# Kernel optimization log

Hardware: AMD Instinct MI355X
Metric: run time of the kernel (lower is better)

The kernel has to match this reference:

```python
import jax, jax.numpy as jnp
import numpy as np

N_NODES = 50000
N_EDGES = 1600000
N_GRAPHS = 64
IN_DIM = 128
HID = 128
N_CLASSES = 10


def setup_inputs() -> dict:
    key = jax.random.key(0)
    ks = jax.random.split(key, 12)
    x = jax.random.normal(ks[0], (N_NODES, IN_DIM), dtype=jnp.float32)
    edge_index = jax.random.randint(ks[1], (2, N_EDGES), 0, N_NODES, dtype=jnp.int32)
    batch = jnp.sort(jax.random.randint(ks[2], (N_NODES,), 0, N_GRAPHS, dtype=jnp.int32))
    def glorot(k, shape):
        s = 1.0 / np.sqrt(shape[0])
        return jax.random.uniform(k, shape, jnp.float32, -s, s)
    W1 = glorot(ks[3], (IN_DIM, HID)); b1 = jnp.zeros((HID,), jnp.float32)
    W2 = glorot(ks[4], (HID, HID));    b2 = jnp.zeros((HID,), jnp.float32)
    Wc1 = glorot(ks[5], (HID, HID));   bc1 = glorot(ks[6], (HID,))
    Wc2 = glorot(ks[7], (HID, N_CLASSES)); bc2 = glorot(ks[8], (N_CLASSES,))
    return {"x": x, "edge_index": edge_index, "batch": batch,
            "W1": W1, "b1": b1, "W2": W2, "b2": b2,
            "Wc1": Wc1, "bc1": bc1, "Wc2": Wc2, "bc2": bc2}


def gcn_conv(x, edge_index, W, b):
    """PyG GCNConv: sym-normalized A-hat (with self loops) @ (x W) + b."""
    n = x.shape[0]
    loop = jnp.arange(n, dtype=edge_index.dtype)
    src = jnp.concatenate([edge_index[0], loop])  # message source
    dst = jnp.concatenate([edge_index[1], loop])  # message target
    deg = jax.ops.segment_sum(jnp.ones_like(src, dtype=x.dtype), dst, num_segments=n)
    dinv = jnp.where(deg > 0, jax.lax.rsqrt(deg), jnp.zeros_like(deg))
    norm = dinv[src] * dinv[dst]  # [E+N]
    h = x @ W                     # [N, H]
    msg = h[src] * norm[:, None]  # gather + scale
    out = jax.ops.segment_sum(msg, dst, num_segments=n)
    return out + b


def reference(x, edge_index, batch, W1, b1, W2, b2, Wc1, bc1, Wc2, bc2):
    h = jax.nn.relu(gcn_conv(x, edge_index, W1, b1))
    h = jax.nn.relu(gcn_conv(h, edge_index, W2, b2))
    # per-graph mean pooling (segment mean)
    sums = jax.ops.segment_sum(h, batch, num_segments=N_GRAPHS)
    cnt = jax.ops.segment_sum(jnp.ones((h.shape[0],), h.dtype), batch, num_segments=N_GRAPHS)
    g = sums / jnp.clip(cnt, 1.0)[:, None]  # [G, H]
    z = jax.nn.relu(g @ Wc1 + bc1)
    return z @ Wc2 + bc2
```

## Files before the change

### kernel.cpp

```cpp
#include <hip/hip_runtime.h>
#include <cstdint>
#include <cstddef>

#define CHUNK 4096

typedef __attribute__((ext_vector_type(8))) short short8;
typedef __attribute__((ext_vector_type(4))) float f32x4;

__device__ __forceinline__ float bf2f(unsigned short u) {
  return __uint_as_float(((unsigned)u) << 16);
}
__device__ __forceinline__ unsigned short f2bf(float f) {
  unsigned u = __float_as_uint(f);
  u += 0x7fffu + ((u >> 16) & 1u);
  return (unsigned short)(u >> 16);
}

__global__ void transpose2_w_k(const float* __restrict__ W1, const float* __restrict__ W2,
                               unsigned short* __restrict__ W1t, unsigned short* __restrict__ W2t) {
  int idx = blockIdx.x * 256 + threadIdx.x;
  const float* W = (idx < 16384) ? W1 : W2;
  unsigned short* Wt = (idx < 16384) ? W1t : W2t;
  int i = idx & 16383;
  int k = i >> 7, n = i & 127;
  Wt[n * 128 + k] = f2bf(W[i]);
}

__global__ void count_edges_k(const int* __restrict__ dst, int E, int* __restrict__ cnt) {
  int e = blockIdx.x * blockDim.x + threadIdx.x;
  if (e < E) atomicAdd(&cnt[dst[e]], 1);
}

__global__ void dinv_k(const int* __restrict__ cnt, float* __restrict__ dinv, int n) {
  int i = blockIdx.x * blockDim.x + threadIdx.x;
  if (i < n) dinv[i] = rsqrtf((float)cnt[i] + 1.0f);
}

template <typename CT>
__global__ void fill_csr_k(const int* __restrict__ src, const int* __restrict__ dst, int E,
                           int* __restrict__ cursor, CT* __restrict__ col) {
  int e = blockIdx.x * blockDim.x + threadIdx.x;
  if (e < E) {
    int d = dst[e], s = src[e];
    int pos = atomicAdd(&cursor[d], 1);
    col[pos] = (CT)s;
  }
}

__global__ void scan1_k(const int* __restrict__ cnt, int* __restrict__ rs,
                        int* __restrict__ partials, int n) {
  __shared__ int s[1024];
  int t = threadIdx.x;
  int gid = blockIdx.x * 1024 + t;
  int v = (gid < n) ? cnt[gid] : 0;
  s[t] = v;
  __syncthreads();
  for (int off = 1; off < 1024; off <<= 1) {
    int u = (t >= off) ? s[t - off] : 0;
    __syncthreads();
    s[t] += u;
    __syncthreads();
  }
  if (gid < n) rs[gid] = s[t] - v;
  if (t == 1023) partials[blockIdx.x] = s[1023];
}

__global__ void scan2_k(int* __restrict__ partials, int nb) {
  if (threadIdx.x == 0 && blockIdx.x == 0) {
    int acc = 0;
    for (int i = 0; i < nb; i++) { int v = partials[i]; partials[i] = acc; acc += v; }
  }
}

__global__ void scan3_k(int* __restrict__ rs, int* __restrict__ cursor,
                        const int* __restrict__ partials, int n, int total) {
  int gid = blockIdx.x * blockDim.x + threadIdx.x;
  if (gid < n) {
    int v = rs[gid] + partials[gid >> 10];
    rs[gid] = v;
    cursor[gid] = v;
  }
  if (gid == 0) rs[n] = total;
}

__global__ __launch_bounds__(256) void scatter_atomic_k(const int* __restrict__ src,
                                                        const int* __restrict__ dst, int E,
                                                        int* __restrict__ gcur,
                                                        unsigned int* __restrict__ tmp,
                                                        int cap, int B) {
  __shared__ unsigned pk[CHUNK];
  __shared__ unsigned char bk[CHUNK];
  __shared__ int h[256];
  __shared__ int cur[256];
  __shared__ int base_s[256];
  int t = threadIdx.x;
  h[t] = 0;
  __syncthreads();
  int e0 = blockIdx.x * CHUNK;
  int e1 = e0 + CHUNK; if (e1 > E) e1 = E;
  int m = e1 - e0;
  for (int i = t; i < m; i += 256) {
    int d = dst[e0 + i], s = src[e0 + i];
    int b = d >> 8;
    pk[i] = ((unsigned)s << 8) | (unsigned)(d & 255);
    bk[i] = (unsigned char)b;
    atomicAdd(&h[b], 1);
  }
  __syncthreads();
  if (t < B && h[t] > 0) base_s[t] = atomicAdd(&gcur[t], h[t]);
  cur[t] = 0;
  __syncthreads();
  for (int i = t; i < m; i += 256) {
    int b = bk[i];
    int r = atomicAdd(&cur[b], 1);
    int p = base_s[b] + r;
    if (p < cap) tmp[(size_t)b * cap + p] = pk[i];
  }
}

__global__ void base2_k(const int* __restrict__ gcur, int B, int cap,
                        int* __restrict__ bucket_base) {
  int lane = threadIdx.x;
  int running = 0;
  for (int c0 = 0; c0 < B; c0 += 64) {
    int idx = c0 + lane;
    int cb = (idx < B) ? gcur[idx] : 0;
    if (cb > cap) cb = cap;
    int v = cb;
    #pragma unroll
    for (int off = 1; off < 64; off <<= 1) {
      int u = __shfl_up(v, off);
      if (lane >= off) v += u;
    }
    int tot = __shfl(v, 63);
    if (idx < B) bucket_base[idx] = running + (v - cb);
    running += tot;
  }
  if (lane == 0) bucket_base[B] = running;
}

__global__ __launch_bounds__(256) void cntfill2_k(const unsigned int* __restrict__ tmp,
                                                  const int* __restrict__ gcur,
                                                  const int* __restrict__ bucket_base,
                                                  int N, int E, int cap,
                                                  float* __restrict__ dinv,
                                                  int* __restrict__ rs,
                                                  unsigned short* __restrict__ col) {
  __shared__ int c[256];
  __shared__ int cur[256];
  int b = blockIdx.x, t = threadIdx.x;
  c[t] = 0;
  __syncthreads();
  int cnt_b = gcur[b]; if (cnt_b > cap) cnt_b = cap;
  const unsigned* tb = tmp + (size_t)b * cap;
  for (int i = t; i < cnt_b; i += 256) atomicAdd(&c[tb[i] & 255u], 1);
  __syncthreads();
  int v = c[t];
  cur[t] = v;
  __syncthreads();
  for (int off = 1; off < 256; off <<= 1) {
    int u = (t >= off) ? cur[t - off] : 0;
    __syncthreads();
    cur[t] += u;
    __syncthreads();
  }
  int rsv = bucket_base[b] + cur[t] - v;
  int node = (b << 8) + t;
  if (node < N) {
    rs[node] = rsv;
    dinv[node] = rsqrtf((float)v + 1.0f);
  }
  if (b == 0 && t == 0) rs[N] = E;
  __syncthreads();
  cur[t] = rsv;
  __syncthreads();
  for (int i = t; i < cnt_b; i += 256) {
    unsigned u = tb[i];
    int pos = atomicAdd(&cur[u & 255u], 1);
    col[pos] = (unsigned short)(u >> 8);
  }
}

template <bool AF32>
__global__ __launch_bounds__(256) void gemm_bf_k(const void* __restrict__ Ap,
                                                 const unsigned short* __restrict__ Wt,
                                                 unsigned short* __restrict__ C, int N) {
  __shared__ unsigned short Ws[128 * 136];
  for (int idx = threadIdx.x; idx < 2048; idx += 256) {
    int n = idx >> 4, c = idx & 15;
    *(uint4*)&Ws[n * 136 + c * 8] = ((const uint4*)Wt)[idx];
  }
  __syncthreads();
  const int w = threadIdx.x >> 6;
  const int lane = threadIdx.x & 63;
  const int quad = lane >> 4, l16 = lane & 15;
  const int rb = blockIdx.x * 128 + w * 32;
  f32x4 acc[2][8] = {};
  #pragma unroll
  for (int ks = 0; ks < 4; ks++) {
    short8 aF[2];
    #pragma unroll
    for (int m = 0; m < 2; m++) {
      int r = rb + m * 16 + l16;
      short8 a = {};
      if (r < N) {
        if (AF32) {
          const float* ar = (const float*)Ap + (size_t)r * 128 + ks * 32 + quad * 8;
          float4 u0 = *(const float4*)ar;
          float4 u1 = *(const float4*)(ar + 4);
          a[0] = (short)f2bf(u0.x); a[1] = (short)f2bf(u0.y);
          a[2] = (short)f2bf(u0.z); a[3] = (short)f2bf(u0.w);
          a[4] = (short)f2bf(u1.x); a[5] = (short)f2bf(u1.y);
          a[6] = (short)f2bf(u1.z); a[7] = (short)f2bf(u1.w);
        } else {
          a = *(const short8*)((const unsigned short*)Ap + (size_t)r * 128 + ks * 32 + quad * 8);
        }
      }
      aF[m] = a;
    }
    #pragma unroll
    for (int t = 0; t < 8; t++) {
      short8 bF = *(const short8*)&Ws[(t * 16 + l16) * 136 + ks * 32 + quad * 8];
      acc[0][t] = __builtin_amdgcn_mfma_f32_16x16x32_bf16(aF[0], bF, acc[0][t], 0, 0, 0);
      acc[1][t] = __builtin_amdgcn_mfma_f32_16x16x32_bf16(aF[1], bF, acc[1][t], 0, 0, 0);
    }
  }
  __syncthreads();
  unsigned short* Cs = Ws;
  #pragma unroll
  for (int m = 0; m < 2; m++) {
    int rloc = w * 32 + m * 16 + quad * 4;
    #pragma unroll
    for (int t = 0; t < 8; t++)
      #pragma unroll
      for (int rg = 0; rg < 4; rg++)
        Cs[(rloc + rg) * 132 + t * 16 + l16] = f2bf(acc[m][t][rg]);
  }
  __syncthreads();
  const int r0 = blockIdx.x * 128;
  for (int idx = threadIdx.x; idx < 2048; idx += 256) {
    int row = idx >> 4, c = idx & 15;
    int rr = r0 + row;
    if (rr < N) {
      uint2 a = *(uint2*)&Cs[row * 132 + c * 8];
      uint2 b = *(uint2*)&Cs[row * 132 + c * 8 + 4];
      ((uint4*)C)[(size_t)rr * 16 + c] = make_uint4(a.x, a.y, b.x, b.y);
    }
  }
}

template <typename CT>
__global__ __launch_bounds__(256) void agg8_k(const unsigned short* __restrict__ h,
                                              const int* __restrict__ rs,
                                              const CT* __restrict__ col,
                                              const float* __restrict__ dinv,
                                              const float* __restrict__ bias,
                                              unsigned short* __restrict__ outp, int n) {
  int wid = (blockIdx.x * blockDim.x + threadIdx.x) >> 6;
  int lane = threadIdx.x & 63;
  if (wid >= n) return;
  const int g = lane >> 4;
  const int l = lane & 15;
  float di = dinv[wid];
  float acc[8];
  {
    uint4 sv = ((const uint4*)(h + (size_t)wid * 128))[l];
    float ws = (g == 0) ? di : 0.f;
    acc[0] = bf2f((unsigned short)sv.x) * ws;
    acc[1] = bf2f((unsigned short)(sv.x >> 16)) * ws;
    acc[2] = bf2f((unsigned short)sv.y) * ws;
    acc[3] = bf2f((unsigned short)(sv.y >> 16)) * ws;
    acc[4] = bf2f((unsigned short)sv.z) * ws;
    acc[5] = bf2f((unsigned short)(sv.z >> 16)) * ws;
    acc[6] = bf2f((unsigned short)sv.w) * ws;
    acc[7] = bf2f((unsigned short)(sv.w >> 16)) * ws;
  }
  int beg = rs[wid], end = rs[wid + 1];
  for (int base = beg; base < end; base += 8) {
    int e0 = base + g, e1 = base + 4 + g;
    int i0 = (e0 < end) ? e0 : end - 1;
    int i1 = (e1 < end) ? e1 : end - 1;
    int s0 = (int)col[i0], s1 = (int)col[i1];
    float w0 = (e0 < end) ? dinv[s0] : 0.f;
    float w1 = (e1 < end) ? dinv[s1] : 0.f;
    uint4 h0 = ((const uint4*)(h + (size_t)s0 * 128))[l];
    uint4 h1 = ((const uint4*)(h + (size_t)s1 * 128))[l];
    acc[0] += bf2f((unsigned short)h0.x) * w0 + bf2f((unsigned short)h1.x) * w1;
    acc[1] += bf2f((unsigned short)(h0.x >> 16)) * w0 + bf2f((unsigned short)(h1.x >> 16)) * w1;
    acc[2] += bf2f((unsigned short)h0.y) * w0 + bf2f((unsigned short)h1.y) * w1;
    acc[3] += bf2f((unsigned short)(h0.y >> 16)) * w0 + bf2f((unsigned short)(h1.y >> 16)) * w1;
    acc[4] += bf2f((unsigned short)h0.z) * w0 + bf2f((unsigned short)h1.z) * w1;
    acc[5] += bf2f((unsigned short)(h0.z >> 16)) * w0 + bf2f((unsigned short)(h1.z >> 16)) * w1;
    acc[6] += bf2f((unsigned short)h0.w) * w0 + bf2f((unsigned short)h1.w) * w1;
    acc[7] += bf2f((unsigned short)(h0.w >> 16)) * w0 + bf2f((unsigned short)(h1.w >> 16)) * w1;
  }
  #pragma unroll
  for (int j = 0; j < 8; j++) {
    acc[j] += __shfl_xor(acc[j], 16);
    acc[j] += __shfl_xor(acc[j], 32);
  }
  if (g == 0) {
    float4 bA = *(const float4*)(bias + l * 8);
    float4 bB = *(const float4*)(bias + l * 8 + 4);
    float r0 = fmaxf(acc[0] * di + bA.x, 0.f);
    float r1 = fmaxf(acc[1] * di + bA.y, 0.f);
    float r2 = fmaxf(acc[2] * di + bA.z, 0.f);
    float r3 = fmaxf(acc[3] * di + bA.w, 0.f);
    float r4 = fmaxf(acc[4] * di + bB.x, 0.f);
    float r5 = fmaxf(acc[5] * di + bB.y, 0.f);
    float r6 = fmaxf(acc[6] * di + bB.z, 0.f);
    float r7 = fmaxf(acc[7] * di + bB.w, 0.f);
    uint4 v;
    v.x = (unsigned)f2bf(r0) | ((unsigned)f2bf(r1) << 16);
    v.y = (unsigned)f2bf(r2) | ((unsigned)f2bf(r3) << 16);
    v.z = (unsigned)f2bf(r4) | ((unsigned)f2bf(r5) << 16);
    v.w = (unsigned)f2bf(r6) | ((unsigned)f2bf(r7) << 16);
    ((uint4*)outp)[(size_t)wid * 16 + l] = v;
  }
}

__global__ void poolb_k(const unsigned short* __restrict__ h, const int* __restrict__ batch, int n,
                        float* __restrict__ pool, float* __restrict__ gcnt) {
  int f = threadIdx.x;
  int n0 = blockIdx.x * 64;
  if (n0 >= n) return;
  int n1 = n0 + 64; if (n1 > n) n1 = n;
  int gcur = batch[n0];
  float acc = 0.f, cacc = 0.f;
  for (int i = n0; i < n1; i++) {
    int g = batch[i];
    if (g != gcur) {
      atomicAdd(&pool[gcur * 128 + f], acc);
      if (f == 0) atomicAdd(&gcnt[gcur], cacc);
      acc = 0.f; cacc = 0.f; gcur = g;
    }
    acc += bf2f(h[(size_t)i * 128 + f]);
    cacc += 1.f;
  }
  atomicAdd(&pool[gcur * 128 + f], acc);
  if (f == 0) atomicAdd(&gcnt[gcur], cacc);
}

__global__ void classify_k(const float* __restrict__ pool, const float* __restrict__ gcnt,
                           const float* __restrict__ Wc1, const float* __restrict__ bc1,
                           const float* __restrict__ Wc2, const float* __restrict__ bc2,
                           float* __restrict__ out, int nc) {
  __shared__ float gs[128];
  __shared__ float zs[128];
  int g = blockIdx.x, t = threadIdx.x;
  float c = gcnt[g]; if (c < 1.f) c = 1.f;
  gs[t] = pool[g * 128 + t] / c;
  __syncthreads();
  float acc = bc1[t];
  for (int k = 0; k < 128; k++) acc += gs[k] * Wc1[k * 128 + t];
  zs[t] = fmaxf(acc, 0.f);
  __syncthreads();
  if (t < nc) {
    float o = bc2[t];
    for (int k = 0; k < 128; k++) o += zs[k] * Wc2[k * nc + t];
    out[g * nc + t] = o;
  }
}

extern "C" void kernel_launch(void* const* d_in, const int* in_sizes, int n_in,
                              void* d_out, int out_size, void* d_ws, size_t ws_size,
                              hipStream_t stream) {
  const float* x   = (const float*)d_in[0];
  const int*   ei  = (const int*)d_in[1];
  const int*   bat = (const int*)d_in[2];
  const float* W1  = (const float*)d_in[3];
  const float* b1  = (const float*)d_in[4];
  const float* W2  = (const float*)d_in[5];
  const float* b2  = (const float*)d_in[6];
  const float* Wc1 = (const float*)d_in[7];
  const float* bc1 = (const float*)d_in[8];
  const float* Wc2 = (const float*)d_in[9];
  const float* bc2 = (const float*)d_in[10];
  float* out = (float*)d_out;

  const int N  = in_sizes[0] / 128;
  const int E  = in_sizes[1] / 2;
  const int NC = in_sizes[10];
  const int G  = out_size / NC;
  const int* src = ei;
  const int* dst = ei + E;
  (void)n_in; (void)ws_size;

  size_t off = 0;
  auto walloc = [&](size_t bytes) -> void* {
    void* p = (char*)d_ws + off;
    off += (bytes + 255) & ~(size_t)255;
    return p;
  };
  unsigned short* B2 = (unsigned short*)walloc((size_t)N * 128 * 2);
  unsigned short* B3 = (unsigned short*)walloc((size_t)N * 128 * 2);
  unsigned short* W1t = (unsigned short*)walloc(128 * 128 * 2);
  unsigned short* W2t = (unsigned short*)walloc(128 * 128 * 2);
  float* dinv = (float*)walloc((size_t)N * 4);
  int*   rs   = (int*)  walloc((size_t)(N + 1) * 4);
  float* pool = (float*)walloc((size_t)G * 129 * 4);
  float* gcnt = pool + (size_t)G * 128;

  const bool small = (N <= 65535);
  const int gblocks = (N + 127) / 128;
  const int aggGrid = (N + 3) / 4;

  transpose2_w_k<<<128, 256, 0, stream>>>(W1, W2, W1t, W2t);

  if (small) {
    const int B    = (N + 255) >> 8;
    const int nblk = (E + CHUNK - 1) / CHUNK;
    const int cap  = (E + B - 1) / B + 2048;
    unsigned short* col = (unsigned short*)walloc((size_t)E * 2);
    unsigned int*   tmp = (unsigned int*)  walloc((size_t)B * cap * 4);
    int* gcur        = (int*)walloc((size_t)B * 4);
    int* bucket_base = (int*)walloc((size_t)(B + 1) * 4);

    hipMemsetAsync(gcur, 0, (size_t)B * 4, stream);
    scatter_atomic_k<<<nblk, 256, 0, stream>>>(src, dst, E, gcur, tmp, cap, B);
    base2_k<<<1, 64, 0, stream>>>(gcur, B, cap, bucket_base);
    cntfill2_k<<<B, 256, 0, stream>>>(tmp, gcur, bucket_base, N, E, cap, dinv, rs, col);

    gemm_bf_k<true><<<gblocks, 256, 0, stream>>>(x, W1t, B2, N);
    agg8_k<unsigned short><<<aggGrid, 256, 0, stream>>>(B2, rs, col, dinv, b1, B3, N);
    gemm_bf_k<false><<<gblocks, 256, 0, stream>>>(B3, W2t, B2, N);
    agg8_k<unsigned short><<<aggGrid, 256, 0, stream>>>(B2, rs, col, dinv, b2, B3, N);
  } else {
    const int nb = (N + 1023) / 1024;
    int* cnt    = (int*)walloc((size_t)N * 4);
    int* cursor = (int*)walloc((size_t)N * 4);
    int* col    = (int*)walloc((size_t)E * 4);
    int* partials = (int*)walloc(256 * 4);
    hipMemsetAsync(cnt, 0, (size_t)N * 4, stream);
    count_edges_k<<<(E + 255) / 256, 256, 0, stream>>>(dst, E, cnt);
    scan1_k<<<nb, 1024, 0, stream>>>(cnt, rs, partials, N);
    scan2_k<<<1, 64, 0, stream>>>(partials, nb);
    scan3_k<<<(N + 255) / 256, 256, 0, stream>>>(rs, cursor, partials, N, E);
    dinv_k<<<(N + 255) / 256, 256, 0, stream>>>(cnt, dinv, N);
    fill_csr_k<int><<<(E + 255) / 256, 256, 0, stream>>>(src, dst, E, cursor, col);

    gemm_bf_k<true><<<gblocks, 256, 0, stream>>>(x, W1t, B2, N);
    agg8_k<int><<<aggGrid, 256, 0, stream>>>(B2, rs, col, dinv, b1, B3, N);
    gemm_bf_k<false><<<gblocks, 256, 0, stream>>>(B3, W2t, B2, N);
    agg8_k<int><<<aggGrid, 256, 0, stream>>>(B2, rs, col, dinv, b2, B3, N);
  }

  hipMemsetAsync(pool, 0, (size_t)G * 129 * 4, stream);
  poolb_k<<<(N + 63) / 64, 128, 0, stream>>>(B3, bat, N, pool, gcnt);
  classify_k<<<G, 128, 0, stream>>>(pool, gcnt, Wc1, bc1, Wc2, bc2, out, NC);
}
```

Before: 314.4 us.

## Fuse CSR finalize, both GCN layers, pooling and classifier into one cooperative kernel

Replaces the chain of separate launches after edge bucketing (base scan, CSR fill, two GEMMs, two aggregations, pooling, classifier) with a single persistent cooperative kernel separated by grid-wide syncs. The weight transpose, bucket-counter reset and pool zeroing are folded into one prep kernel, replacing the memsets. The bucket-base scan is recomputed in every block. The aim is to remove launch overhead and inter-kernel gaps, at the cost of grid barriers and of grid-stride loops that may under-fill the device in some phases.

```diff
diff --git a/kernel.cpp b/kernel.cpp
--- a/kernel.cpp
+++ b/kernel.cpp
@@ -1,6 +1,9 @@
 #include <hip/hip_runtime.h>
+#include <hip/hip_cooperative_groups.h>
 #include <cstdint>
 #include <cstddef>
+
+namespace cg = cooperative_groups;
 
 #define CHUNK 4096
 
@@ -16,71 +19,18 @@
   return (unsigned short)(u >> 16);
 }
 
-__global__ void transpose2_w_k(const float* __restrict__ W1, const float* __restrict__ W2,
-                               unsigned short* __restrict__ W1t, unsigned short* __restrict__ W2t) {
+__global__ void prep_k(const float* __restrict__ W1, const float* __restrict__ W2,
+                       unsigned short* __restrict__ W1t, unsigned short* __restrict__ W2t,
+                       int* __restrict__ gcur, int B, float* __restrict__ pool, int poolN) {
   int idx = blockIdx.x * 256 + threadIdx.x;
   const float* W = (idx < 16384) ? W1 : W2;
   unsigned short* Wt = (idx < 16384) ? W1t : W2t;
   int i = idx & 16383;
   int k = i >> 7, n = i & 127;
   Wt[n * 128 + k] = f2bf(W[i]);
-}
-
-__global__ void count_edges_k(const int* __restrict__ dst, int E, int* __restrict__ cnt) {
-  int e = blockIdx.x * blockDim.x + threadIdx.x;
-  if (e < E) atomicAdd(&cnt[dst[e]], 1);
-}
-
-__global__ void dinv_k(const int* __restrict__ cnt, float* __restrict__ dinv, int n) {
-  int i = blockIdx.x * blockDim.x + threadIdx.x;
-  if (i < n) dinv[i] = rsqrtf((float)cnt[i] + 1.0f);
-}
-
-template <typename CT>
-__global__ void fill_csr_k(const int* __restrict__ src, const int* __restrict__ dst, int E,
-                           int* __restrict__ cursor, CT* __restrict__ col) {
-  int e = blockIdx.x * blockDim.x + threadIdx.x;
-  if (e < E) {
-    int d = dst[e], s = src[e];
-    int pos = atomicAdd(&cursor[d], 1);
-    col[pos] = (CT)s;
-  }
-}
-
-__global__ void scan1_k(const int* __restrict__ cnt, int* __restrict__ rs,
-                        int* __restrict__ partials, int n) {
-  __shared__ int s[1024];
-  int t = threadIdx.x;
-  int gid = blockIdx.x * 1024 + t;
-  int v = (gid < n) ? cnt[gid] : 0;
-  s[t] = v;
-  __syncthreads();
-  for (int off = 1; off < 1024; off <<= 1) {
-    int u = (t >= off) ? s[t - off] : 0;
-    __syncthreads();
-    s[t] += u;
-    __syncthreads();
-  }
-  if (gid < n) rs[gid] = s[t] - v;
-  if (t == 1023) partials[blockIdx.x] = s[1023];
-}
-
-__global__ void scan2_k(int* __restrict__ partials, int nb) {
-  if (threadIdx.x == 0 && blockIdx.x == 0) {
-    int acc = 0;
-    for (int i = 0; i < nb; i++) { int v = partials[i]; partials[i] = acc; acc += v; }
-  }
-}
-
-__global__ void scan3_k(int* __restrict__ rs, int* __restrict__ cursor,
-                        const int* __restrict__ partials, int n, int total) {
-  int gid = blockIdx.x * blockDim.x + threadIdx.x;
-  if (gid < n) {
-    int v = rs[gid] + partials[gid >> 10];
-    rs[gid] = v;
-    cursor[gid] = v;
-  }
-  if (gid == 0) rs[n] = total;
+  if (blockIdx.x == 0 && threadIdx.x < B) gcur[threadIdx.x] = 0;
+  if (blockIdx.x == 127)
+    for (int j = threadIdx.x; j < poolN; j += 256) pool[j] = 0.f;
 }
 
 __global__ __launch_bounds__(256) void scatter_atomic_k(const int* __restrict__ src,
@@ -118,83 +68,38 @@
   }
 }
 
-__global__ void base2_k(const int* __restrict__ gcur, int B, int cap,
-                        int* __restrict__ bucket_base) {
-  int lane = threadIdx.x;
-  int running = 0;
-  for (int c0 = 0; c0 < B; c0 += 64) {
-    int idx = c0 + lane;
-    int cb = (idx < B) ? gcur[idx] : 0;
-    if (cb > cap) cb = cap;
-    int v = cb;
-    #pragma unroll
-    for (int off = 1; off < 64; off <<= 1) {
-      int u = __shfl_up(v, off);
-      if (lane >= off) v += u;
-    }
-    int tot = __shfl(v, 63);
-    if (idx < B) bucket_base[idx] = running + (v - cb);
-    running += tot;
-  }
-  if (lane == 0) bucket_base[B] = running;
-}
-
-__global__ __launch_bounds__(256) void cntfill2_k(const unsigned int* __restrict__ tmp,
-                                                  const int* __restrict__ gcur,
-                                                  const int* __restrict__ bucket_base,
-                                                  int N, int E, int cap,
-                                                  float* __restrict__ dinv,
-                                                  int* __restrict__ rs,
-                                                  unsigned short* __restrict__ col) {
-  __shared__ int c[256];
-  __shared__ int cur[256];
-  int b = blockIdx.x, t = threadIdx.x;
-  c[t] = 0;
-  __syncthreads();
-  int cnt_b = gcur[b]; if (cnt_b > cap) cnt_b = cap;
-  const unsigned* tb = tmp + (size_t)b * cap;
-  for (int i = t; i < cnt_b; i += 256) atomicAdd(&c[tb[i] & 255u], 1);
-  __syncthreads();
-  int v = c[t];
-  cur[t] = v;
-  __syncthreads();
-  for (int off = 1; off < 256; off <<= 1) {
-    int u = (t >= off) ? cur[t - off] : 0;
-    __syncthreads();
-    cur[t] += u;
-    __syncthreads();
-  }
-  int rsv = bucket_base[b] + cur[t] - v;
-  int node = (b << 8) + t;
-  if (node < N) {
-    rs[node] = rsv;
-    dinv[node] = rsqrtf((float)v + 1.0f);
-  }
-  if (b == 0 && t == 0) rs[N] = E;
-  __syncthreads();
-  cur[t] = rsv;
-  __syncthreads();
-  for (int i = t; i < cnt_b; i += 256) {
-    unsigned u = tb[i];
-    int pos = atomicAdd(&cur[u & 255u], 1);
-    col[pos] = (unsigned short)(u >> 8);
-  }
-}
+struct CoopArgs {
+  const float* x;
+  const unsigned short* W1t; const unsigned short* W2t;
+  const float* b1; const float* b2;
+  const int* gcur; const unsigned* tmp; int cap; int B;
+  float* dinv; int* rs; unsigned short* col;
+  unsigned short* B2; unsigned short* B3;
+  const int* bat; float* pool; float* gcnt;
+  const float* Wc1; const float* bc1; const float* Wc2; const float* bc2;
+  float* out;
+  int N; int E; int NC; int G; int ntiles; int naggq;
+};
+
+union SMem {
+  unsigned short ws[128 * 136];
+  struct { int c[256]; int cur[256]; int sb[256]; } cf;
+  struct { float gs[128]; float zs[128]; } cl;
+};
 
 template <bool AF32>
-__global__ __launch_bounds__(256) void gemm_bf_k(const void* __restrict__ Ap,
-                                                 const unsigned short* __restrict__ Wt,
-                                                 unsigned short* __restrict__ C, int N) {
-  __shared__ unsigned short Ws[128 * 136];
+__device__ __forceinline__ void gemm_tile(SMem& sm, const void* Ap,
+                                          const unsigned short* Wt,
+                                          unsigned short* C, int N, int tile) {
   for (int idx = threadIdx.x; idx < 2048; idx += 256) {
     int n = idx >> 4, c = idx & 15;
-    *(uint4*)&Ws[n * 136 + c * 8] = ((const uint4*)Wt)[idx];
+    *(uint4*)&sm.ws[n * 136 + c * 8] = ((const uint4*)Wt)[idx];
   }
   __syncthreads();
   const int w = threadIdx.x >> 6;
   const int lane = threadIdx.x & 63;
   const int quad = lane >> 4, l16 = lane & 15;
-  const int rb = blockIdx.x * 128 + w * 32;
+  const int rb = tile * 128 + w * 32;
   f32x4 acc[2][8] = {};
   #pragma unroll
   for (int ks = 0; ks < 4; ks++) {
@@ -220,13 +125,13 @@
     }
     #pragma unroll
     for (int t = 0; t < 8; t++) {
-      short8 bF = *(const short8*)&Ws[(t * 16 + l16) * 136 + ks * 32 + quad * 8];
+      short8 bF = *(const short8*)&sm.ws[(t * 16 + l16) * 136 + ks * 32 + quad * 8];
       acc[0][t] = __builtin_amdgcn_mfma_f32_16x16x32_bf16(aF[0], bF, acc[0][t], 0, 0, 0);
       acc[1][t] = __builtin_amdgcn_mfma_f32_16x16x32_bf16(aF[1], bF, acc[1][t], 0, 0, 0);
     }
   }
   __syncthreads();
-  unsigned short* Cs = Ws;
+  unsigned short* Cs = sm.ws;
   #pragma unroll
   for (int m = 0; m < 2; m++) {
     int rloc = w * 32 + m * 16 + quad * 4;
@@ -237,7 +142,7 @@
         Cs[(rloc + rg) * 132 + t * 16 + l16] = f2bf(acc[m][t][rg]);
   }
   __syncthreads();
-  const int r0 = blockIdx.x * 128;
+  const int r0 = tile * 128;
   for (int idx = threadIdx.x; idx < 2048; idx += 256) {
     int row = idx >> 4, c = idx & 15;
     int rr = r0 + row;
@@ -247,18 +152,13 @@
       ((uint4*)C)[(size_t)rr * 16 + c] = make_uint4(a.x, a.y, b.x, b.y);
     }
   }
-}
-
-template <typename CT>
-__global__ __launch_bounds__(256) void agg8_k(const unsigned short* __restrict__ h,
-                                              const int* __restrict__ rs,
-                                              const CT* __restrict__ col,
-                                              const float* __restrict__ dinv,
-                                              const float* __restrict__ bias,
-                                              unsigned short* __restrict__ outp, int n) {
-  int wid = (blockIdx.x * blockDim.x + threadIdx.x) >> 6;
-  int lane = threadIdx.x & 63;
-  if (wid >= n) return;
+  __syncthreads();
+}
+
+__device__ __forceinline__ void agg_node(const unsigned short* h, const int* rs,
+                                         const unsigned short* col, const float* dinv,
+                                         const float* bias, unsigned short* outp,
+                                         int n, int wid, int lane) {
   const int g = lane >> 4;
   const int l = lane & 15;
   float di = dinv[wid];
@@ -319,6 +219,236 @@
   }
 }
 
+__global__ __launch_bounds__(256, 4) void coop_k(CoopArgs a) {
+  cg::grid_group gg = cg::this_grid();
+  __shared__ SMem sm;
+  const int t = threadIdx.x;
+
+  if ((int)blockIdx.x < a.B) {
+    int b = blockIdx.x;
+    int cb = 0;
+    if (t < a.B) { cb = a.gcur[t]; if (cb > a.cap) cb = a.cap; }
+    sm.cf.sb[t] = cb;
+    __syncthreads();
+    for (int off = 1; off < 256; off <<= 1) {
+      int u = (t >= off) ? sm.cf.sb[t - off] : 0;
+      __syncthreads();
+      sm.cf.sb[t] += u;
+      __syncthreads();
+    }
+    int base_b = (b > 0) ? sm.cf.sb[b - 1] : 0;
+    int cnt_b = sm.cf.sb[b] - base_b;
+    if (b == 0 && t == 0) a.rs[a.N] = sm.cf.sb[a.B - 1];
+    const unsigned* tb = a.tmp + (size_t)b * a.cap;
+    sm.cf.c[t] = 0;
+    __syncthreads();
+    for (int i = t; i < cnt_b; i += 256) atomicAdd(&sm.cf.c[tb[i] & 255u], 1);
+    __syncthreads();
+    int v = sm.cf.c[t];
+    sm.cf.cur[t] = v;
+    __syncthreads();
+    for (int off = 1; off < 256; off <<= 1) {
+      int u = (t >= off) ? sm.cf.cur[t - off] : 0;
+      __syncthreads();
+      sm.cf.cur[t] += u;
+      __syncthreads();
+    }
+    int rsv = base_b + sm.cf.cur[t] - v;
+    int node = (b << 8) + t;
+    if (node < a.N) {
+      a.rs[node] = rsv;
+      a.dinv[node] = rsqrtf((float)v + 1.0f);
+    }
+    __syncthreads();
+    sm.cf.cur[t] = rsv;
+    __syncthreads();
+    for (int i = t; i < cnt_b; i += 256) {
+      unsigned u = tb[i];
+      int pos = atomicAdd(&sm.cf.cur[u & 255u], 1);
+      a.col[pos] = (unsigned short)(u >> 8);
+    }
+  }
+  gg.sync();
+
+  for (int tile = blockIdx.x; tile < a.ntiles; tile += gridDim.x)
+    gemm_tile<true>(sm, a.x, a.W1t, a.B2, a.N, tile);
+  gg.sync();
+
+  {
+    int lane = t & 63, wv = t >> 6;
+    for (int q = blockIdx.x; q < a.naggq; q += gridDim.x) {
+      int wid = q * 4 + wv;
+      if (wid < a.N) agg_node(a.B2, a.rs, a.col, a.dinv, a.b1, a.B3, a.N, wid, lane);
+    }
+  }
+  gg.sync();
+
+  for (int tile = blockIdx.x; tile < a.ntiles; tile += gridDim.x)
+    gemm_tile<false>(sm, a.B3, a.W2t, a.B2, a.N, tile);
+  gg.sync();
+
+  {
+    int lane = t & 63, wv = t >> 6;
+    for (int q = blockIdx.x; q < a.naggq; q += gridDim.x) {
+      int wid = q * 4 + wv;
+      if (wid < a.N) agg_node(a.B2, a.rs, a.col, a.dinv, a.b2, a.B3, a.N, wid, lane);
+    }
+  }
+  gg.sync();
+
+  {
+    int hf = t >> 7;
+    int f = t & 127;
+    int nchunks = (a.N + 63) / 64;
+    for (int c = blockIdx.x * 2 + hf; c < nchunks; c += gridDim.x * 2) {
+      int n0 = c * 64;
+      int n1 = n0 + 64; if (n1 > a.N) n1 = a.N;
+      int gcur_ = a.bat[n0];
+      float acc = 0.f, cacc = 0.f;
+      for (int i = n0; i < n1; i++) {
+        int g = a.bat[i];
+        if (g != gcur_) {
+          atomicAdd(&a.pool[gcur_ * 128 + f], acc);
+          if (f == 0) atomicAdd(&a.gcnt[gcur_], cacc);
+          acc = 0.f; cacc = 0.f; gcur_ = g;
+        }
+        acc += bf2f(a.B3[(size_t)i * 128 + f]);
+        cacc += 1.f;
+      }
+      atomicAdd(&a.pool[gcur_ * 128 + f], acc);
+      if (f == 0) atomicAdd(&a.gcnt[gcur_], cacc);
+    }
+  }
+  gg.sync();
+
+  if ((int)blockIdx.x < a.G) {
+    int g = blockIdx.x;
+    if (t < 128) {
+      float c = a.gcnt[g]; if (c < 1.f) c = 1.f;
+      sm.cl.gs[t] = a.pool[g * 128 + t] / c;
+    }
+    __syncthreads();
+    if (t < 128) {
+      float acc = a.bc1[t];
+      for (int k = 0; k < 128; k++) acc += sm.cl.gs[k] * a.Wc1[k * 128 + t];
+      sm.cl.zs[t] = fmaxf(acc, 0.f);
+    }
+    __syncthreads();
+    if (t < a.NC) {
+      float o = a.bc2[t];
+      for (int k = 0; k < 128; k++) o += sm.cl.zs[k] * a.Wc2[k * a.NC + t];
+      a.out[g * a.NC + t] = o;
+    }
+  }
+}
+
+__global__ void count_edges_k(const int* __restrict__ dst, int E, int* __restrict__ cnt) {
+  int e = blockIdx.x * blockDim.x + threadIdx.x;
+  if (e < E) atomicAdd(&cnt[dst[e]], 1);
+}
+__global__ void dinv_k(const int* __restrict__ cnt, float* __restrict__ dinv, int n) {
+  int i = blockIdx.x * blockDim.x + threadIdx.x;
+  if (i < n) dinv[i] = rsqrtf((float)cnt[i] + 1.0f);
+}
+__global__ void fill_csr_k(const int* __restrict__ src, const int* __restrict__ dst, int E,
+                           int* __restrict__ cursor, int* __restrict__ col) {
+  int e = blockIdx.x * blockDim.x + threadIdx.x;
+  if (e < E) {
+    int d = dst[e], s = src[e];
+    int pos = atomicAdd(&cursor[d], 1);
+    col[pos] = s;
+  }
+}
+__global__ void scan1_k(const int* __restrict__ cnt, int* __restrict__ rs,
+                        int* __restrict__ partials, int n) {
+  __shared__ int s[1024];
+  int t = threadIdx.x;
+  int gid = blockIdx.x * 1024 + t;
+  int v = (gid < n) ? cnt[gid] : 0;
+  s[t] = v;
+  __syncthreads();
+  for (int off = 1; off < 1024; off <<= 1) {
+    int u = (t >= off) ? s[t - off] : 0;
+    __syncthreads();
+    s[t] += u;
+    __syncthreads();
+  }
+  if (gid < n) rs[gid] = s[t] - v;
+  if (t == 1023) partials[blockIdx.x] = s[1023];
+}
+__global__ void scan2_k(int* __restrict__ partials, int nb) {
+  if (threadIdx.x == 0 && blockIdx.x == 0) {
+    int acc = 0;
+    for (int i = 0; i < nb; i++) { int v = partials[i]; partials[i] = acc; acc += v; }
+  }
+}
+__global__ void scan3_k(int* __restrict__ rs, int* __restrict__ cursor,
+                        const int* __restrict__ partials, int n, int total) {
+  int gid = blockIdx.x * blockDim.x + threadIdx.x;
+  if (gid < n) {
+    int v = rs[gid] + partials[gid >> 10];
+    rs[gid] = v;
+    cursor[gid] = v;
+  }
+  if (gid == 0) rs[n] = total;
+}
+template <bool AF32>
+__global__ __launch_bounds__(256) void gemm_bf_k(const void* __restrict__ Ap,
+                                                 const unsigned short* __restrict__ Wt,
+                                                 unsigned short* __restrict__ C, int N) {
+  __shared__ SMem sm;
+  gemm_tile<AF32>(sm, Ap, Wt, C, N, blockIdx.x);
+}
+__global__ __launch_bounds__(256) void agg8i_k(const unsigned short* __restrict__ h,
+                                               const int* __restrict__ rs,
+                                               const int* __restrict__ col,
+                                               const float* __restrict__ dinv,
+                                               const float* __restrict__ bias,
+                                               unsigned short* __restrict__ outp, int n) {
+  int wid = (blockIdx.x * blockDim.x + threadIdx.x) >> 6;
+  int lane = threadIdx.x & 63;
+  if (wid >= n) return;
+  const int g = lane >> 4, l = lane & 15;
+  float di = dinv[wid];
+  float acc[8];
+  uint4 sv = ((const uint4*)(h + (size_t)wid * 128))[l];
+  float ws = (g == 0) ? di : 0.f;
+  acc[0] = bf2f((unsigned short)sv.x) * ws; acc[1] = bf2f((unsigned short)(sv.x >> 16)) * ws;
+  acc[2] = bf2f((unsigned short)sv.y) * ws; acc[3] = bf2f((unsigned short)(sv.y >> 16)) * ws;
+  acc[4] = bf2f((unsigned short)sv.z) * ws; acc[5] = bf2f((unsigned short)(sv.z >> 16)) * ws;
+  acc[6] = bf2f((unsigned short)sv.w) * ws; acc[7] = bf2f((unsigned short)(sv.w >> 16)) * ws;
+  int beg = rs[wid], end = rs[wid + 1];
+  for (int base = beg; base < end; base += 8) {
+    int e0 = base + g, e1 = base + 4 + g;
+    int i0 = (e0 < end) ? e0 : end - 1;
+    int i1 = (e1 < end) ? e1 : end - 1;
+    int s0 = col[i0], s1 = col[i1];
+    float w0 = (e0 < end) ? dinv[s0] : 0.f;
+    float w1 = (e1 < end) ? dinv[s1] : 0.f;
+    uint4 h0 = ((const uint4*)(h + (size_t)s0 * 128))[l];
+    uint4 h1 = ((const uint4*)(h + (size_t)s1 * 128))[l];
+    acc[0] += bf2f((unsigned short)h0.x) * w0 + bf2f((unsigned short)h1.x) * w1;
+    acc[1] += bf2f((unsigned short)(h0.x >> 16)) * w0 + bf2f((unsigned short)(h1.x >> 16)) * w1;
+    acc[2] += bf2f((unsigned short)h0.y) * w0 + bf2f((unsigned short)h1.y) * w1;
+    acc[3] += bf2f((unsigned short)(h0.y >> 16)) * w0 + bf2f((unsigned short)(h1.y >> 16)) * w1;
+    acc[4] += bf2f((unsigned short)h0.z) * w0 + bf2f((unsigned short)h1.z) * w1;
+    acc[5] += bf2f((unsigned short)(h0.z >> 16)) * w0 + bf2f((unsigned short)(h1.z >> 16)) * w1;
+    acc[6] += bf2f((unsigned short)h0.w) * w0 + bf2f((unsigned short)h1.w) * w1;
+    acc[7] += bf2f((unsigned short)(h0.w >> 16)) * w0 + bf2f((unsigned short)(h1.w >> 16)) * w1;
+  }
+  #pragma unroll
+  for (int j = 0; j < 8; j++) { acc[j] += __shfl_xor(acc[j], 16); acc[j] += __shfl_xor(acc[j], 32); }
+  if (g == 0) {
+    float4 bA = *(const float4*)(bias + l * 8);
+    float4 bB = *(const float4*)(bias + l * 8 + 4);
+    uint4 v;
+    v.x = (unsigned)f2bf(fmaxf(acc[0] * di + bA.x, 0.f)) | ((unsigned)f2bf(fmaxf(acc[1] * di + bA.y, 0.f)) << 16);
+    v.y = (unsigned)f2bf(fmaxf(acc[2] * di + bA.z, 0.f)) | ((unsigned)f2bf(fmaxf(acc[3] * di + bA.w, 0.f)) << 16);
+    v.z = (unsigned)f2bf(fmaxf(acc[4] * di + bB.x, 0.f)) | ((unsigned)f2bf(fmaxf(acc[5] * di + bB.y, 0.f)) << 16);
+    v.w = (unsigned)f2bf(fmaxf(acc[6] * di + bB.z, 0.f)) | ((unsigned)f2bf(fmaxf(acc[7] * di + bB.w, 0.f)) << 16);
+    ((uint4*)outp)[(size_t)wid * 16 + l] = v;
+  }
+}
 __global__ void poolb_k(const unsigned short* __restrict__ h, const int* __restrict__ batch, int n,
                         float* __restrict__ pool, float* __restrict__ gcnt) {
   int f = threadIdx.x;
@@ -340,7 +470,6 @@
   atomicAdd(&pool[gcur * 128 + f], acc);
   if (f == 0) atomicAdd(&gcnt[gcur], cacc);
 }
-
 __global__ void classify_k(const float* __restrict__ pool, const float* __restrict__ gcnt,
                            const float* __restrict__ Wc1, const float* __restrict__ bc1,
                            const float* __restrict__ Wc2, const float* __restrict__ bc2,
@@ -402,10 +531,6 @@
   float* gcnt = pool + (size_t)G * 128;
 
   const bool small = (N <= 65535);
-  const int gblocks = (N + 127) / 128;
-  const int aggGrid = (N + 3) / 4;
-
-  transpose2_w_k<<<128, 256, 0, stream>>>(W1, W2, W1t, W2t);
 
   if (small) {
     const int B    = (N + 255) >> 8;
@@ -413,39 +538,57 @@
     const int cap  = (E + B - 1) / B + 2048;
     unsigned short* col = (unsigned short*)walloc((size_t)E * 2);
     unsigned int*   tmp = (unsigned int*)  walloc((size_t)B * cap * 4);
-    int* gcur        = (int*)walloc((size_t)B * 4);
-    int* bucket_base = (int*)walloc((size_t)(B + 1) * 4);
-
-    hipMemsetAsync(gcur, 0, (size_t)B * 4, stream);
+    int* gcur = (int*)walloc((size_t)B * 4);
+
+    prep_k<<<128, 256, 0, stream>>>(W1, W2, W1t, W2t, gcur, B, pool, G * 129);
     scatter_atomic_k<<<nblk, 256, 0, stream>>>(src, dst, E, gcur, tmp, cap, B);
-    base2_k<<<1, 64, 0, stream>>>(gcur, B, cap, bucket_base);
-    cntfill2_k<<<B, 256, 0, stream>>>(tmp, gcur, bucket_base, N, E, cap, dinv, rs, col);
-
-    gemm_bf_k<true><<<gblocks, 256, 0, stream>>>(x, W1t, B2, N);
-    agg8_k<unsigned short><<<aggGrid, 256, 0, stream>>>(B2, rs, col, dinv, b1, B3, N);
-    gemm_bf_k<false><<<gblocks, 256, 0, stream>>>(B3, W2t, B2, N);
-    agg8_k<unsigned short><<<aggGrid, 256, 0, stream>>>(B2, rs, col, dinv, b2, B3, N);
+
+    CoopArgs ca;
+    ca.x = x; ca.W1t = W1t; ca.W2t = W2t; ca.b1 = b1; ca.b2 = b2;
+    ca.gcur = gcur; ca.tmp = tmp; ca.cap = cap; ca.B = B;
+    ca.dinv = dinv; ca.rs = rs; ca.col = col;
+    ca.B2 = B2; ca.B3 = B3;
+    ca.bat = bat; ca.pool = pool; ca.gcnt = gcnt;
+    ca.Wc1 = Wc1; ca.bc1 = bc1; ca.Wc2 = Wc2; ca.bc2 = bc2;
+    ca.out = out;
+    ca.N = N; ca.E = E; ca.NC = NC; ca.G = G;
+    ca.ntiles = (N + 127) / 128;
+    ca.naggq = (N + 3) / 4;
+
+    int nbpc = 0;
+    hipOccupancyMaxActiveBlocksPerMultiprocessor(&nbpc, (const void*)coop_k, 256, 0);
+    if (nbpc < 1) nbpc = 1;
+    int numCU = 0;
+    hipDeviceGetAttribute(&numCU, hipDeviceAttributeMultiprocessorCount, 0);
+    if (numCU < 1) numCU = 256;
+    int grid = nbpc * numCU;
+    if (grid < B) grid = B;
+    if (grid < G) grid = G;
+    void* args[] = { &ca };
+    hipLaunchCooperativeKernel((const void*)coop_k, dim3(grid), dim3(256), args, 0, stream);
   } else {
     const int nb = (N + 1023) / 1024;
+    const int gblocks = (N + 127) / 128;
+    const int aggGrid = (N + 3) / 4;
     int* cnt    = (int*)walloc((size_t)N * 4);
     int* cursor = (int*)walloc((size_t)N * 4);
     int* col    = (int*)walloc((size_t)E * 4);
     int* partials = (int*)walloc(256 * 4);
+    prep_k<<<128, 256, 0, stream>>>(W1, W2, W1t, W2t, cnt , 0, pool, G * 129);
     hipMemsetAsync(cnt, 0, (size_t)N * 4, stream);
     count_edges_k<<<(E + 255) / 256, 256, 0, stream>>>(dst, E, cnt);
     scan1_k<<<nb, 1024, 0, stream>>>(cnt, rs, partials, N);
     scan2_k<<<1, 64, 0, stream>>>(partials, nb);
     scan3_k<<<(N + 255) / 256, 256, 0, stream>>>(rs, cursor, partials, N, E);
     dinv_k<<<(N + 255) / 256, 256, 0, stream>>>(cnt, dinv, N);
-    fill_csr_k<int><<<(E + 255) / 256, 256, 0, stream>>>(src, dst, E, cursor, col);
+    fill_csr_k<<<(E + 255) / 256, 256, 0, stream>>>(src, dst, E, cursor, (int*)col);
 
     gemm_bf_k<true><<<gblocks, 256, 0, stream>>>(x, W1t, B2, N);
-    agg8_k<int><<<aggGrid, 256, 0, stream>>>(B2, rs, col, dinv, b1, B3, N);
+    agg8i_k<<<aggGrid, 256, 0, stream>>>(B2, rs, (int*)col, dinv, b1, B3, N);
     gemm_bf_k<false><<<gblocks, 256, 0, stream>>>(B3, W2t, B2, N);
-    agg8_k<int><<<aggGrid, 256, 0, stream>>>(B2, rs, col, dinv, b2, B3, N);
-  }
-
-  hipMemsetAsync(pool, 0, (size_t)G * 129 * 4, stream);
-  poolb_k<<<(N + 63) / 64, 128, 0, stream>>>(B3, bat, N, pool, gcnt);
-  classify_k<<<G, 128, 0, stream>>>(pool, gcnt, Wc1, bc1, Wc2, bc2, out, NC);
-}
+    agg8i_k<<<aggGrid, 256, 0, stream>>>(B2, rs, (int*)col, dinv, b2, B3, N);
+
+    poolb_k<<<(N + 63) / 64, 128, 0, stream>>>(B3, bat, N, pool, gcnt);
+    classify_k<<<G, 128, 0, stream>>>(pool, gcnt, Wc1, bc1, Wc2, bc2, out, NC);
+  }
+}
```

Result: slower. 827.4 us (+163.2%).
